# Kernel tuning notes

Measured on AMD Instinct MI355X. Metric: run time of the kernel, lower is better.

The kernel has to match this reference:

```python
import jax, jax.numpy as jnp
import numpy as np

N_NODES = 100000
N_RELS = 4
N_EDGES = 250000  # per relation
D = 128


def setup_inputs() -> dict:
    key = jax.random.key(0)
    ks = jax.random.split(key, 7)
    scale = 1.0 / np.sqrt(D)  # xavier-like scaling for stability
    x = jax.random.normal(ks[0], (N_NODES, D), dtype=jnp.float32)
    weight = jax.random.normal(ks[1], (N_RELS, D, D), dtype=jnp.float32) * scale
    conv_bias = jax.random.normal(ks[2], (N_RELS, D), dtype=jnp.float32) * 0.1
    loop_weight = jax.random.normal(ks[3], (D, D), dtype=jnp.float32) * scale
    node_bias = jax.random.normal(ks[4], (1, D), dtype=jnp.float32) * 0.1
    src = jax.random.randint(ks[5], (N_RELS, N_EDGES), 0, N_NODES)
    dst = jax.random.randint(ks[6], (N_RELS, N_EDGES), 0, N_NODES)
    return {"x": x, "weight": weight, "conv_bias": conv_bias,
            "loop_weight": loop_weight, "node_bias": node_bias,
            "src": src, "dst": dst}


def reference(x, weight, conv_bias, loop_weight, node_bias, src, dst):
    N = x.shape[0]

    def per_rel(s, d, W, b):
        # GraphConv(norm='right'): sum src feats into dst, divide by in-degree (clamped to 1),
        # then matmul weight (aggregate-first since in_feat == out_feat), add bias, activation.
        msg = jax.ops.segment_sum(x[s], d, num_segments=N)              # [N, D]
        deg = jax.ops.segment_sum(jnp.ones(s.shape, x.dtype), d, num_segments=N)
        h = (msg / jnp.maximum(deg, 1.0)[:, None]) @ W + b              # [N, D]
        return jax.nn.relu(h)

    hs = jax.vmap(per_rel)(src, dst, weight, conv_bias)                 # [R, N, D]
    h = hs.mean(axis=0)                                                 # HeteroGraphConv aggregate='mean'
    h = h * jax.nn.sigmoid(h)                                           # GLU(tile(h, 2)) == SiLU(h)
    h = h + x @ loop_weight + node_bias                                  # self-loop + ntype bias
    return jax.nn.relu(h)                                                # dropout=0 (eval)
```

## Files before the change

kernel.cpp:

```cpp
#include <hip/hip_runtime.h>
#include <hip/hip_bf16.h>

#define N_NODES 100000
#define N_RELS  4
#define N_EDGES 250000
#define TOTAL_E (N_RELS * N_EDGES)
#define NR      (N_RELS * N_NODES)
#define D       128

typedef __attribute__((ext_vector_type(8))) short bf16x8;
typedef __attribute__((ext_vector_type(4))) float f32x4;

__device__ __forceinline__ float b2f(short u) {
    unsigned int x = ((unsigned int)(unsigned short)u) << 16;
    return __builtin_bit_cast(float, x);
}
__device__ __forceinline__ unsigned short f2b(float f) {
    unsigned int u = __builtin_bit_cast(unsigned int, f);
    return (unsigned short)((u + 0x7fffu + ((u >> 16) & 1u)) >> 16);
}

#define PREP_X_BLKS 6250
#define PREP_W_BLKS 320
#define PREP_H_BLKS 3907
__global__ __launch_bounds__(256) void prep_kernel(
    const float* __restrict__ x, const float* __restrict__ weight,
    const float* __restrict__ loop_w, const int* __restrict__ dst,
    unsigned short* __restrict__ xb, unsigned short* __restrict__ wT,
    int* __restrict__ deg)
{
    int b = blockIdx.x, t = threadIdx.x;
    if (b < PREP_X_BLKS) {
        int i = b * 256 + t;
        float4 v0 = *reinterpret_cast<const float4*>(x + (size_t)i * 8);
        float4 v1 = *reinterpret_cast<const float4*>(x + (size_t)i * 8 + 4);
        bf16x8 o;
        o[0] = (short)f2b(v0.x); o[1] = (short)f2b(v0.y);
        o[2] = (short)f2b(v0.z); o[3] = (short)f2b(v0.w);
        o[4] = (short)f2b(v1.x); o[5] = (short)f2b(v1.y);
        o[6] = (short)f2b(v1.z); o[7] = (short)f2b(v1.w);
        *reinterpret_cast<bf16x8*>(xb + (size_t)i * 8) = o;
    } else if (b < PREP_X_BLKS + PREP_W_BLKS) {
        int i = (b - PREP_X_BLKS) * 256 + t;
        int mat = i >> 14;
        int n   = (i >> 7) & 127;
        int k   = i & 127;
        const float* srcm = (mat < 4) ? (weight + (size_t)mat * D * D) : loop_w;
        wT[i] = f2b(srcm[k * D + n]);
    } else {
        int i = (b - PREP_X_BLKS - PREP_W_BLKS) * 256 + t;
        if (i < TOTAL_E) {
            int rel = i / N_EDGES;
            atomicAdd(&deg[rel * N_NODES + dst[i]], 1);
        }
    }
}

__global__ __launch_bounds__(256) void scan1_kernel(
    const int* __restrict__ in, int* __restrict__ out,
    int* __restrict__ aux, int n)
{
    __shared__ int s[256];
    int t = threadIdx.x;
    int base = blockIdx.x * 1024 + t * 4;
    int v[4];
    int sum = 0;
    #pragma unroll
    for (int j = 0; j < 4; ++j) {
        v[j] = (base + j < n) ? in[base + j] : 0;
        sum += v[j];
    }
    s[t] = sum;
    for (int off = 1; off < 256; off <<= 1) {
        __syncthreads();
        int u = (t >= off) ? s[t - off] : 0;
        __syncthreads();
        s[t] += u;
    }
    __syncthreads();
    int excl = (t > 0) ? s[t - 1] : 0;
    #pragma unroll
    for (int j = 0; j < 4; ++j) {
        if (base + j < n) out[base + j] = excl;
        excl += v[j];
    }
    if (t == 255) aux[blockIdx.x] = s[255];
}

__global__ __launch_bounds__(256) void addoff2_kernel(
    int* __restrict__ off, int* __restrict__ cursor,
    const int* __restrict__ aux, int n)
{
    __shared__ int sred[256];
    int c = blockIdx.x, t = threadIdx.x;
    if (c == 0 && t == 0) off[NR] = TOTAL_E;
    int part = 0;
    for (int j = t; j < c; j += 256) part += aux[j];
    sred[t] = part;
    for (int o = 128; o > 0; o >>= 1) {
        __syncthreads();
        if (t < o) sred[t] += sred[t + o];
    }
    __syncthreads();
    int S = sred[0];
    int base = c * 1024 + t * 4;
    #pragma unroll
    for (int j = 0; j < 4; ++j) {
        int i = base + j;
        if (i < n) { int v = off[i] + S; off[i] = v; cursor[i] = v; }
    }
}

__global__ __launch_bounds__(256) void fill_kernel(
    const int* __restrict__ dst, const int* __restrict__ src,
    int* __restrict__ cursor, int* __restrict__ sorted_src, int total)
{
    int i = blockIdx.x * 256 + threadIdx.x;
    if (i >= total) return;
    int rel = i / N_EDGES;
    int pos = atomicAdd(&cursor[rel * N_NODES + dst[i]], 1);
    sorted_src[pos] = src[i];
}

__global__ __launch_bounds__(256) void fused_gemm_mfma(
    const unsigned short* __restrict__ xb,
    const unsigned short* __restrict__ wT,
    const float* __restrict__ conv_bias,
    const float* __restrict__ node_bias,
    const int* __restrict__ off,
    const int* __restrict__ sorted_src,
    float* __restrict__ out)
{
    __shared__ __align__(16) unsigned char sIn[32 * 256];

    const int tid  = threadIdx.x;
    const int row0 = blockIdx.x * 32;
    const int wid  = tid >> 6;
    const int lane = tid & 63;
    const int l15  = lane & 15;
    const int l4   = lane >> 4;
    const int swA  = (l15 & 7) << 4;

    const int gr  = tid >> 3;
    const int gc  = tid & 7;
    const int gsw = (gr & 7) << 4;

    f32x4 acc_mean[2][2];
    f32x4 acc_self[2][2];
    #pragma unroll
    for (int m = 0; m < 2; ++m)
        #pragma unroll
        for (int n = 0; n < 2; ++n)
            acc_mean[m][n] = (f32x4){0.f, 0.f, 0.f, 0.f};

    for (int phase = 0; phase < 4; ++phase) {
        __syncthreads();

        {
            int node = phase * N_NODES + row0 + gr;
            int beg  = off[node];
            int dgi  = off[node + 1] - beg;
            const int* sp = sorted_src + beg;
            const unsigned short* xcol = xb + gc * 16;

            float a[16];
            #pragma unroll
            for (int j = 0; j < 16; ++j) a[j] = 0.f;

            int e = 0;
            for (; e + 4 <= dgi; e += 4) {
                int s0 = sp[e], s1 = sp[e + 1], s2 = sp[e + 2], s3 = sp[e + 3];
                const bf16x8* p0 = reinterpret_cast<const bf16x8*>(xcol + (size_t)s0 * D);
                const bf16x8* p1 = reinterpret_cast<const bf16x8*>(xcol + (size_t)s1 * D);
                const bf16x8* p2 = reinterpret_cast<const bf16x8*>(xcol + (size_t)s2 * D);
                const bf16x8* p3 = reinterpret_cast<const bf16x8*>(xcol + (size_t)s3 * D);
                bf16x8 u0 = p0[0], w0 = p0[1];
                bf16x8 u1 = p1[0], w1 = p1[1];
                bf16x8 u2 = p2[0], w2 = p2[1];
                bf16x8 u3 = p3[0], w3 = p3[1];
                #pragma unroll
                for (int j = 0; j < 8; ++j) {
                    a[j]     += b2f(u0[j]) + b2f(u1[j]) + b2f(u2[j]) + b2f(u3[j]);
                    a[8 + j] += b2f(w0[j]) + b2f(w1[j]) + b2f(w2[j]) + b2f(w3[j]);
                }
            }
            for (; e < dgi; ++e) {
                const bf16x8* p = reinterpret_cast<const bf16x8*>(xcol + (size_t)sp[e] * D);
                bf16x8 u = p[0], w = p[1];
                #pragma unroll
                for (int j = 0; j < 8; ++j) {
                    a[j]     += b2f(u[j]);
                    a[8 + j] += b2f(w[j]);
                }
            }

            float scl = 1.0f / fmaxf((float)dgi, 1.0f);
            bf16x8 o0, o1;
            #pragma unroll
            for (int j = 0; j < 8; ++j) {
                o0[j] = (short)f2b(a[j] * scl);
                o1[j] = (short)f2b(a[8 + j] * scl);
            }
            int base = gr * 256;
            *reinterpret_cast<bf16x8*>(&sIn[base + ((gc * 32) ^ gsw)])      = o0;
            *reinterpret_cast<bf16x8*>(&sIn[base + ((gc * 32 + 16) ^ gsw)]) = o1;
        }
        __syncthreads();

        const unsigned short* wp = wT + (size_t)phase * D * D;
        f32x4 acc[2][2];
        #pragma unroll
        for (int m = 0; m < 2; ++m)
            #pragma unroll
            for (int n = 0; n < 2; ++n)
                acc[m][n] = (f32x4){0.f, 0.f, 0.f, 0.f};

        #pragma unroll
        for (int s = 0; s < 4; ++s) {
            int kb = s * 64 + l4 * 16;
            bf16x8 a0 = *reinterpret_cast<const bf16x8*>(
                &sIn[l15 * 256 + (kb ^ swA)]);
            bf16x8 a1 = *reinterpret_cast<const bf16x8*>(
                &sIn[(16 + l15) * 256 + (kb ^ swA)]);
            bf16x8 b0 = *reinterpret_cast<const bf16x8*>(
                wp + (wid * 32 + l15) * D + s * 32 + l4 * 8);
            bf16x8 b1 = *reinterpret_cast<const bf16x8*>(
                wp + (wid * 32 + 16 + l15) * D + s * 32 + l4 * 8);
            acc[0][0] = __builtin_amdgcn_mfma_f32_16x16x32_bf16(a0, b0, acc[0][0], 0, 0, 0);
            acc[0][1] = __builtin_amdgcn_mfma_f32_16x16x32_bf16(a0, b1, acc[0][1], 0, 0, 0);
            acc[1][0] = __builtin_amdgcn_mfma_f32_16x16x32_bf16(a1, b0, acc[1][0], 0, 0, 0);
            acc[1][1] = __builtin_amdgcn_mfma_f32_16x16x32_bf16(a1, b1, acc[1][1], 0, 0, 0);
        }

        float b0 = conv_bias[phase * D + wid * 32 + l15];
        float b1 = conv_bias[phase * D + wid * 32 + 16 + l15];
        #pragma unroll
        for (int m = 0; m < 2; ++m)
            #pragma unroll
            for (int j = 0; j < 4; ++j) {
                acc_mean[m][0][j] += 0.25f * fmaxf(acc[m][0][j] + b0, 0.f);
                acc_mean[m][1][j] += 0.25f * fmaxf(acc[m][1][j] + b1, 0.f);
            }
    }

    {
        const unsigned short* wp = wT + (size_t)4 * D * D;
        f32x4 acc[2][2];
        #pragma unroll
        for (int m = 0; m < 2; ++m)
            #pragma unroll
            for (int n = 0; n < 2; ++n)
                acc[m][n] = (f32x4){0.f, 0.f, 0.f, 0.f};

        #pragma unroll
        for (int s = 0; s < 4; ++s) {
            bf16x8 a0 = *reinterpret_cast<const bf16x8*>(
                xb + (size_t)(row0 + l15) * D + s * 32 + l4 * 8);
            bf16x8 a1 = *reinterpret_cast<const bf16x8*>(
                xb + (size_t)(row0 + 16 + l15) * D + s * 32 + l4 * 8);
            bf16x8 b0 = *reinterpret_cast<const bf16x8*>(
                wp + (wid * 32 + l15) * D + s * 32 + l4 * 8);
            bf16x8 b1 = *reinterpret_cast<const bf16x8*>(
                wp + (wid * 32 + 16 + l15) * D + s * 32 + l4 * 8);
            acc[0][0] = __builtin_amdgcn_mfma_f32_16x16x32_bf16(a0, b0, acc[0][0], 0, 0, 0);
            acc[0][1] = __builtin_amdgcn_mfma_f32_16x16x32_bf16(a0, b1, acc[0][1], 0, 0, 0);
            acc[1][0] = __builtin_amdgcn_mfma_f32_16x16x32_bf16(a1, b0, acc[1][0], 0, 0, 0);
            acc[1][1] = __builtin_amdgcn_mfma_f32_16x16x32_bf16(a1, b1, acc[1][1], 0, 0, 0);
        }
        float b0 = node_bias[wid * 32 + l15];
        float b1 = node_bias[wid * 32 + 16 + l15];
        #pragma unroll
        for (int m = 0; m < 2; ++m)
            #pragma unroll
            for (int j = 0; j < 4; ++j) {
                acc_self[m][0][j] = acc[m][0][j] + b0;
                acc_self[m][1][j] = acc[m][1][j] + b1;
            }
    }

    #pragma unroll
    for (int m = 0; m < 2; ++m)
        #pragma unroll
        for (int n = 0; n < 2; ++n)
            #pragma unroll
            for (int j = 0; j < 4; ++j) {
                float mn = acc_mean[m][n][j];
                float sl = mn / (1.0f + __expf(-mn));
                float v  = fmaxf(sl + acc_self[m][n][j], 0.f);
                int row = row0 + m * 16 + l4 * 4 + j;
                int col = wid * 32 + n * 16 + l15;
                out[(size_t)row * D + col] = v;
            }
}

extern "C" void kernel_launch(void* const* d_in, const int* in_sizes, int n_in,
                              void* d_out, int out_size, void* d_ws, size_t ws_size,
                              hipStream_t stream) {
    const float* x         = (const float*)d_in[0];
    const float* weight    = (const float*)d_in[1];
    const float* conv_bias = (const float*)d_in[2];
    const float* loop_w    = (const float*)d_in[3];
    const float* node_bias = (const float*)d_in[4];
    const int*   src       = (const int*)d_in[5];
    const int*   dst       = (const int*)d_in[6];
    float* out = (float*)d_out;

    char* w = (char*)d_ws;
    int* deg            = (int*)(w);
    int* off            = (int*)(w + 1600000);
    int* cursor         = (int*)(w + 3200008);
    int* aux            = (int*)(w + 4800008);
    int* sorted_src     = (int*)(w + 4802056);
    unsigned short* xb  = (unsigned short*)(w + 8802056);
    unsigned short* wT  = (unsigned short*)(w + 8802056 + (size_t)N_NODES * D * 2);

    const int SCAN_BLKS = (NR + 1023) / 1024;

    hipMemsetAsync(deg, 0, NR * sizeof(int), stream);
    prep_kernel<<<PREP_X_BLKS + PREP_W_BLKS + PREP_H_BLKS, 256, 0, stream>>>(
        x, weight, loop_w, dst, xb, wT, deg);
    scan1_kernel<<<SCAN_BLKS, 256, 0, stream>>>(deg, off, aux, NR);
    addoff2_kernel<<<SCAN_BLKS, 256, 0, stream>>>(off, cursor, aux, NR);
    fill_kernel<<<(TOTAL_E + 255) / 256, 256, 0, stream>>>(
        dst, src, cursor, sorted_src, TOTAL_E);
    fused_gemm_mfma<<<N_NODES / 32, 256, 0, stream>>>(
        xb, wT, conv_bias, node_bias, off, sorted_src, out);
}
```

Baseline: 356.9 us.

## Shrink fused GEMM to one wave per 16-row tile with hoisted offsets

The fused gather-plus-MFMA kernel now uses single-wavefront blocks, each handling 16 nodes instead of 32. Each lane gathers 32 columns of one node rather than 16, and that wave computes all 128 output columns with 8 MFMA accumulators. Offsets for all four relations are loaded up front. This creates twice as many, lighter blocks and makes the block barriers cheap, but each wave now loads every weight tile itself and needs more registers.

```diff
diff --git a/kernel.cpp b/kernel.cpp
--- a/kernel.cpp
+++ b/kernel.cpp
@@ -122,7 +122,7 @@
     sorted_src[pos] = src[i];
 }
 
-__global__ __launch_bounds__(256) void fused_gemm_mfma(
+__global__ __launch_bounds__(64) void fused_gemm_mfma(
     const unsigned short* __restrict__ xb,
     const unsigned short* __restrict__ wT,
     const float* __restrict__ conv_bias,
@@ -131,166 +131,147 @@
     const int* __restrict__ sorted_src,
     float* __restrict__ out)
 {
-    __shared__ __align__(16) unsigned char sIn[32 * 256];
-
-    const int tid  = threadIdx.x;
-    const int row0 = blockIdx.x * 32;
-    const int wid  = tid >> 6;
-    const int lane = tid & 63;
+    __shared__ __align__(16) unsigned char sIn[16 * 256];
+
+    const int lane = threadIdx.x;
+    const int row0 = blockIdx.x * 16;
     const int l15  = lane & 15;
     const int l4   = lane >> 4;
     const int swA  = (l15 & 7) << 4;
 
-    const int gr  = tid >> 3;
-    const int gc  = tid & 7;
+    const int gr  = lane >> 2;
+    const int gc  = lane & 3;
     const int gsw = (gr & 7) << 4;
 
-    f32x4 acc_mean[2][2];
-    f32x4 acc_self[2][2];
-    #pragma unroll
-    for (int m = 0; m < 2; ++m)
-        #pragma unroll
-        for (int n = 0; n < 2; ++n)
-            acc_mean[m][n] = (f32x4){0.f, 0.f, 0.f, 0.f};
+    int begs[4], ends[4];
+    #pragma unroll
+    for (int p = 0; p < 4; ++p) {
+        int node = p * N_NODES + row0 + gr;
+        begs[p] = off[node];
+        ends[p] = off[node + 1];
+    }
+
+    f32x4 acc_mean[8];
+    #pragma unroll
+    for (int n = 0; n < 8; ++n) acc_mean[n] = (f32x4){0.f, 0.f, 0.f, 0.f};
 
     for (int phase = 0; phase < 4; ++phase) {
         __syncthreads();
 
         {
-            int node = phase * N_NODES + row0 + gr;
-            int beg  = off[node];
-            int dgi  = off[node + 1] - beg;
-            const int* sp = sorted_src + beg;
-            const unsigned short* xcol = xb + gc * 16;
-
-            float a[16];
-            #pragma unroll
-            for (int j = 0; j < 16; ++j) a[j] = 0.f;
-
-            int e = 0;
-            for (; e + 4 <= dgi; e += 4) {
-                int s0 = sp[e], s1 = sp[e + 1], s2 = sp[e + 2], s3 = sp[e + 3];
+            int beg = begs[phase], end = ends[phase];
+            const unsigned short* xcol = xb + gc * 32;
+            float a[32];
+            #pragma unroll
+            for (int j = 0; j < 32; ++j) a[j] = 0.f;
+
+            int e = beg;
+            for (; e + 2 <= end; e += 2) {
+                int s0 = sorted_src[e], s1 = sorted_src[e + 1];
                 const bf16x8* p0 = reinterpret_cast<const bf16x8*>(xcol + (size_t)s0 * D);
                 const bf16x8* p1 = reinterpret_cast<const bf16x8*>(xcol + (size_t)s1 * D);
-                const bf16x8* p2 = reinterpret_cast<const bf16x8*>(xcol + (size_t)s2 * D);
-                const bf16x8* p3 = reinterpret_cast<const bf16x8*>(xcol + (size_t)s3 * D);
-                bf16x8 u0 = p0[0], w0 = p0[1];
-                bf16x8 u1 = p1[0], w1 = p1[1];
-                bf16x8 u2 = p2[0], w2 = p2[1];
-                bf16x8 u3 = p3[0], w3 = p3[1];
+                bf16x8 u0 = p0[0], u1 = p0[1], u2 = p0[2], u3 = p0[3];
+                bf16x8 v0 = p1[0], v1 = p1[1], v2 = p1[2], v3 = p1[3];
                 #pragma unroll
                 for (int j = 0; j < 8; ++j) {
-                    a[j]     += b2f(u0[j]) + b2f(u1[j]) + b2f(u2[j]) + b2f(u3[j]);
-                    a[8 + j] += b2f(w0[j]) + b2f(w1[j]) + b2f(w2[j]) + b2f(w3[j]);
+                    a[j]      += b2f(u0[j]) + b2f(v0[j]);
+                    a[8 + j]  += b2f(u1[j]) + b2f(v1[j]);
+                    a[16 + j] += b2f(u2[j]) + b2f(v2[j]);
+                    a[24 + j] += b2f(u3[j]) + b2f(v3[j]);
                 }
             }
-            for (; e < dgi; ++e) {
-                const bf16x8* p = reinterpret_cast<const bf16x8*>(xcol + (size_t)sp[e] * D);
-                bf16x8 u = p[0], w = p[1];
+            if (e < end) {
+                int s0 = sorted_src[e];
+                const bf16x8* p0 = reinterpret_cast<const bf16x8*>(xcol + (size_t)s0 * D);
+                bf16x8 u0 = p0[0], u1 = p0[1], u2 = p0[2], u3 = p0[3];
                 #pragma unroll
                 for (int j = 0; j < 8; ++j) {
-                    a[j]     += b2f(u[j]);
-                    a[8 + j] += b2f(w[j]);
+                    a[j]      += b2f(u0[j]);
+                    a[8 + j]  += b2f(u1[j]);
+                    a[16 + j] += b2f(u2[j]);
+                    a[24 + j] += b2f(u3[j]);
                 }
             }
 
-            float scl = 1.0f / fmaxf((float)dgi, 1.0f);
-            bf16x8 o0, o1;
-            #pragma unroll
-            for (int j = 0; j < 8; ++j) {
-                o0[j] = (short)f2b(a[j] * scl);
-                o1[j] = (short)f2b(a[8 + j] * scl);
-            }
-            int base = gr * 256;
-            *reinterpret_cast<bf16x8*>(&sIn[base + ((gc * 32) ^ gsw)])      = o0;
-            *reinterpret_cast<bf16x8*>(&sIn[base + ((gc * 32 + 16) ^ gsw)]) = o1;
+            float scl = 1.0f / fmaxf((float)(end - beg), 1.0f);
+            #pragma unroll
+            for (int q = 0; q < 4; ++q) {
+                bf16x8 o;
+                #pragma unroll
+                for (int j = 0; j < 8; ++j) o[j] = (short)f2b(a[q * 8 + j] * scl);
+                *reinterpret_cast<bf16x8*>(
+                    &sIn[gr * 256 + ((gc * 64 + q * 16) ^ gsw)]) = o;
+            }
         }
         __syncthreads();
 
         const unsigned short* wp = wT + (size_t)phase * D * D;
-        f32x4 acc[2][2];
-        #pragma unroll
-        for (int m = 0; m < 2; ++m)
-            #pragma unroll
-            for (int n = 0; n < 2; ++n)
-                acc[m][n] = (f32x4){0.f, 0.f, 0.f, 0.f};
+        float cb[8];
+        #pragma unroll
+        for (int n = 0; n < 8; ++n)
+            cb[n] = conv_bias[phase * D + n * 16 + l15];
+
+        f32x4 acc[8];
+        #pragma unroll
+        for (int n = 0; n < 8; ++n) acc[n] = (f32x4){0.f, 0.f, 0.f, 0.f};
 
         #pragma unroll
         for (int s = 0; s < 4; ++s) {
-            int kb = s * 64 + l4 * 16;
             bf16x8 a0 = *reinterpret_cast<const bf16x8*>(
-                &sIn[l15 * 256 + (kb ^ swA)]);
-            bf16x8 a1 = *reinterpret_cast<const bf16x8*>(
-                &sIn[(16 + l15) * 256 + (kb ^ swA)]);
-            bf16x8 b0 = *reinterpret_cast<const bf16x8*>(
-                wp + (wid * 32 + l15) * D + s * 32 + l4 * 8);
-            bf16x8 b1 = *reinterpret_cast<const bf16x8*>(
-                wp + (wid * 32 + 16 + l15) * D + s * 32 + l4 * 8);
-            acc[0][0] = __builtin_amdgcn_mfma_f32_16x16x32_bf16(a0, b0, acc[0][0], 0, 0, 0);
-            acc[0][1] = __builtin_amdgcn_mfma_f32_16x16x32_bf16(a0, b1, acc[0][1], 0, 0, 0);
-            acc[1][0] = __builtin_amdgcn_mfma_f32_16x16x32_bf16(a1, b0, acc[1][0], 0, 0, 0);
-            acc[1][1] = __builtin_amdgcn_mfma_f32_16x16x32_bf16(a1, b1, acc[1][1], 0, 0, 0);
-        }
-
-        float b0 = conv_bias[phase * D + wid * 32 + l15];
-        float b1 = conv_bias[phase * D + wid * 32 + 16 + l15];
-        #pragma unroll
-        for (int m = 0; m < 2; ++m)
-            #pragma unroll
-            for (int j = 0; j < 4; ++j) {
-                acc_mean[m][0][j] += 0.25f * fmaxf(acc[m][0][j] + b0, 0.f);
-                acc_mean[m][1][j] += 0.25f * fmaxf(acc[m][1][j] + b1, 0.f);
-            }
-    }
-
+                &sIn[l15 * 256 + ((s * 64 + l4 * 16) ^ swA)]);
+            #pragma unroll
+            for (int n = 0; n < 8; ++n) {
+                bf16x8 b0 = *reinterpret_cast<const bf16x8*>(
+                    wp + (n * 16 + l15) * D + s * 32 + l4 * 8);
+                acc[n] = __builtin_amdgcn_mfma_f32_16x16x32_bf16(a0, b0, acc[n], 0, 0, 0);
+            }
+        }
+
+        #pragma unroll
+        for (int n = 0; n < 8; ++n)
+            #pragma unroll
+            for (int j = 0; j < 4; ++j)
+                acc_mean[n][j] += 0.25f * fmaxf(acc[n][j] + cb[n], 0.f);
+    }
+
+    f32x4 acc_self[8];
     {
         const unsigned short* wp = wT + (size_t)4 * D * D;
-        f32x4 acc[2][2];
-        #pragma unroll
-        for (int m = 0; m < 2; ++m)
-            #pragma unroll
-            for (int n = 0; n < 2; ++n)
-                acc[m][n] = (f32x4){0.f, 0.f, 0.f, 0.f};
+        float nb[8];
+        #pragma unroll
+        for (int n = 0; n < 8; ++n) nb[n] = node_bias[n * 16 + l15];
+        #pragma unroll
+        for (int n = 0; n < 8; ++n) acc_self[n] = (f32x4){0.f, 0.f, 0.f, 0.f};
 
         #pragma unroll
         for (int s = 0; s < 4; ++s) {
             bf16x8 a0 = *reinterpret_cast<const bf16x8*>(
                 xb + (size_t)(row0 + l15) * D + s * 32 + l4 * 8);
-            bf16x8 a1 = *reinterpret_cast<const bf16x8*>(
-                xb + (size_t)(row0 + 16 + l15) * D + s * 32 + l4 * 8);
-            bf16x8 b0 = *reinterpret_cast<const bf16x8*>(
-                wp + (wid * 32 + l15) * D + s * 32 + l4 * 8);
-            bf16x8 b1 = *reinterpret_cast<const bf16x8*>(
-                wp + (wid * 32 + 16 + l15) * D + s * 32 + l4 * 8);
-            acc[0][0] = __builtin_amdgcn_mfma_f32_16x16x32_bf16(a0, b0, acc[0][0], 0, 0, 0);
-            acc[0][1] = __builtin_amdgcn_mfma_f32_16x16x32_bf16(a0, b1, acc[0][1], 0, 0, 0);
-            acc[1][0] = __builtin_amdgcn_mfma_f32_16x16x32_bf16(a1, b0, acc[1][0], 0, 0, 0);
-            acc[1][1] = __builtin_amdgcn_mfma_f32_16x16x32_bf16(a1, b1, acc[1][1], 0, 0, 0);
-        }
-        float b0 = node_bias[wid * 32 + l15];
-        float b1 = node_bias[wid * 32 + 16 + l15];
-        #pragma unroll
-        for (int m = 0; m < 2; ++m)
-            #pragma unroll
-            for (int j = 0; j < 4; ++j) {
-                acc_self[m][0][j] = acc[m][0][j] + b0;
-                acc_self[m][1][j] = acc[m][1][j] + b1;
-            }
-    }
-
-    #pragma unroll
-    for (int m = 0; m < 2; ++m)
-        #pragma unroll
-        for (int n = 0; n < 2; ++n)
-            #pragma unroll
-            for (int j = 0; j < 4; ++j) {
-                float mn = acc_mean[m][n][j];
-                float sl = mn / (1.0f + __expf(-mn));
-                float v  = fmaxf(sl + acc_self[m][n][j], 0.f);
-                int row = row0 + m * 16 + l4 * 4 + j;
-                int col = wid * 32 + n * 16 + l15;
-                out[(size_t)row * D + col] = v;
-            }
+            #pragma unroll
+            for (int n = 0; n < 8; ++n) {
+                bf16x8 b0 = *reinterpret_cast<const bf16x8*>(
+                    wp + (n * 16 + l15) * D + s * 32 + l4 * 8);
+                acc_self[n] = __builtin_amdgcn_mfma_f32_16x16x32_bf16(a0, b0, acc_self[n], 0, 0, 0);
+            }
+        }
+        #pragma unroll
+        for (int n = 0; n < 8; ++n)
+            #pragma unroll
+            for (int j = 0; j < 4; ++j)
+                acc_self[n][j] += nb[n];
+    }
+
+    #pragma unroll
+    for (int n = 0; n < 8; ++n)
+        #pragma unroll
+        for (int j = 0; j < 4; ++j) {
+            float mn = acc_mean[n][j];
+            float sl = mn / (1.0f + __expf(-mn));
+            float v  = fmaxf(sl + acc_self[n][j], 0.f);
+            int row = row0 + l4 * 4 + j;
+            int col = n * 16 + l15;
+            out[(size_t)row * D + col] = v;
+        }
 }
 
 extern "C" void kernel_launch(void* const* d_in, const int* in_sizes, int n_in,
@@ -323,6 +304,6 @@
     addoff2_kernel<<<SCAN_BLKS, 256, 0, stream>>>(off, cursor, aux, NR);
     fill_kernel<<<(TOTAL_E + 255) / 256, 256, 0, stream>>>(
         dst, src, cursor, sorted_src, TOTAL_E);
-    fused_gemm_mfma<<<N_NODES / 32, 256, 0, stream>>>(
+    fused_gemm_mfma<<<N_NODES / 16, 64, 0, stream>>>(
         xb, wT, conv_bias, node_bias, off, sorted_src, out);
 }
```

New measurement: 377.6 us. +5.8%, slower.

## Fuse CSR build into persistent grid-barrier kernel; gather all relations upfront

Applied to the files above, without the earlier changes.

Replaces the memset plus four preprocessing kernels with one persistent kernel of 1024 blocks that uses a software grid barrier between the degree count, scan, offset add and fill stages. This removes launch gaps and tail effects between small kernels. The main kernel now gathers all four relations' neighbour features in one interleaved loop, which raises memory-level parallelism. It then runs the four relation GEMMs from a 4x larger shared buffer without per-phase syncs. The grid barrier relies on all 1024 blocks being co-resident, which is a deadlock risk, and the larger LDS buffer and register arrays may reduce occupancy.

```diff
diff --git a/kernel.cpp b/kernel.cpp
--- a/kernel.cpp
+++ b/kernel.cpp
@@ -7,6 +7,8 @@
 #define TOTAL_E (N_RELS * N_EDGES)
 #define NR      (N_RELS * N_NODES)
 #define D       128
+#define CSR_BLKS 1024
+#define SCAN_BLKS 391
 
 typedef __attribute__((ext_vector_type(8))) short bf16x8;
 typedef __attribute__((ext_vector_type(4))) float f32x4;
@@ -20,18 +22,40 @@
     return (unsigned short)((u + 0x7fffu + ((u >> 16) & 1u)) >> 16);
 }
 
-#define PREP_X_BLKS 6250
-#define PREP_W_BLKS 320
-#define PREP_H_BLKS 3907
-__global__ __launch_bounds__(256) void prep_kernel(
+__device__ __forceinline__ void grid_barrier(int* cnt, int* gen) {
+    __syncthreads();
+    __threadfence();
+    if (threadIdx.x == 0) {
+        int my = __hip_atomic_load(gen, __ATOMIC_RELAXED, __HIP_MEMORY_SCOPE_AGENT);
+        int t  = __hip_atomic_fetch_add(cnt, 1, __ATOMIC_ACQ_REL, __HIP_MEMORY_SCOPE_AGENT);
+        if (t == CSR_BLKS - 1) {
+            __hip_atomic_store(cnt, 0, __ATOMIC_RELAXED, __HIP_MEMORY_SCOPE_AGENT);
+            __hip_atomic_fetch_add(gen, 1, __ATOMIC_RELEASE, __HIP_MEMORY_SCOPE_AGENT);
+        } else {
+            while (__hip_atomic_load(gen, __ATOMIC_ACQUIRE, __HIP_MEMORY_SCOPE_AGENT) == my)
+                __builtin_amdgcn_s_sleep(8);
+        }
+    }
+    __syncthreads();
+    __threadfence();
+}
+
+__global__ __launch_bounds__(256, 4) void csr_prep_kernel(
     const float* __restrict__ x, const float* __restrict__ weight,
-    const float* __restrict__ loop_w, const int* __restrict__ dst,
+    const float* __restrict__ loop_w, const int* __restrict__ src,
+    const int* __restrict__ dst,
     unsigned short* __restrict__ xb, unsigned short* __restrict__ wT,
-    int* __restrict__ deg)
+    int* __restrict__ deg, int* __restrict__ off, int* __restrict__ cursor,
+    int* __restrict__ aux, int* __restrict__ sorted_src,
+    int* __restrict__ bar_cnt, int* __restrict__ bar_gen)
 {
-    int b = blockIdx.x, t = threadIdx.x;
-    if (b < PREP_X_BLKS) {
-        int i = b * 256 + t;
+    const int t   = threadIdx.x;
+    const int gid = blockIdx.x * 256 + t;
+    const int NT  = CSR_BLKS * 256;
+    __shared__ int s[256];
+
+    for (int i = gid; i < NR; i += NT) deg[i] = 0;
+    for (int i = gid; i < N_NODES * D / 8; i += NT) {
         float4 v0 = *reinterpret_cast<const float4*>(x + (size_t)i * 8);
         float4 v1 = *reinterpret_cast<const float4*>(x + (size_t)i * 8 + 4);
         bf16x8 o;
@@ -40,86 +64,71 @@
         o[4] = (short)f2b(v1.x); o[5] = (short)f2b(v1.y);
         o[6] = (short)f2b(v1.z); o[7] = (short)f2b(v1.w);
         *reinterpret_cast<bf16x8*>(xb + (size_t)i * 8) = o;
-    } else if (b < PREP_X_BLKS + PREP_W_BLKS) {
-        int i = (b - PREP_X_BLKS) * 256 + t;
-        int mat = i >> 14;
-        int n   = (i >> 7) & 127;
-        int k   = i & 127;
+    }
+    for (int i = gid; i < 5 * D * D; i += NT) {
+        int mat = i >> 14, n = (i >> 7) & 127, k = i & 127;
         const float* srcm = (mat < 4) ? (weight + (size_t)mat * D * D) : loop_w;
         wT[i] = f2b(srcm[k * D + n]);
-    } else {
-        int i = (b - PREP_X_BLKS - PREP_W_BLKS) * 256 + t;
-        if (i < TOTAL_E) {
-            int rel = i / N_EDGES;
-            atomicAdd(&deg[rel * N_NODES + dst[i]], 1);
-        }
-    }
-}
-
-__global__ __launch_bounds__(256) void scan1_kernel(
-    const int* __restrict__ in, int* __restrict__ out,
-    int* __restrict__ aux, int n)
-{
-    __shared__ int s[256];
-    int t = threadIdx.x;
-    int base = blockIdx.x * 1024 + t * 4;
-    int v[4];
-    int sum = 0;
-    #pragma unroll
-    for (int j = 0; j < 4; ++j) {
-        v[j] = (base + j < n) ? in[base + j] : 0;
-        sum += v[j];
-    }
-    s[t] = sum;
-    for (int off = 1; off < 256; off <<= 1) {
+    }
+    grid_barrier(bar_cnt, bar_gen);
+
+    for (int i = gid; i < TOTAL_E; i += NT) {
+        int rel = i / N_EDGES;
+        atomicAdd(&deg[rel * N_NODES + dst[i]], 1);
+    }
+    grid_barrier(bar_cnt, bar_gen);
+
+    if (blockIdx.x < SCAN_BLKS) {
+        int base = blockIdx.x * 1024 + t * 4;
+        int v[4]; int sum = 0;
+        #pragma unroll
+        for (int j = 0; j < 4; ++j) {
+            v[j] = (base + j < NR) ? deg[base + j] : 0;
+            sum += v[j];
+        }
+        s[t] = sum;
+        for (int o = 1; o < 256; o <<= 1) {
+            __syncthreads();
+            int u = (t >= o) ? s[t - o] : 0;
+            __syncthreads();
+            s[t] += u;
+        }
         __syncthreads();
-        int u = (t >= off) ? s[t - off] : 0;
+        int excl = (t > 0) ? s[t - 1] : 0;
+        #pragma unroll
+        for (int j = 0; j < 4; ++j) {
+            if (base + j < NR) off[base + j] = excl;
+            excl += v[j];
+        }
+        if (t == 255) aux[blockIdx.x] = s[255];
+    }
+    grid_barrier(bar_cnt, bar_gen);
+
+    if (blockIdx.x < SCAN_BLKS) {
+        if (blockIdx.x == 0 && t == 0) off[NR] = TOTAL_E;
+        int part = 0;
+        for (int j = t; j < (int)blockIdx.x; j += 256) part += aux[j];
+        s[t] = part;
+        for (int o = 128; o > 0; o >>= 1) {
+            __syncthreads();
+            if (t < o) s[t] += s[t + o];
+        }
         __syncthreads();
-        s[t] += u;
-    }
-    __syncthreads();
-    int excl = (t > 0) ? s[t - 1] : 0;
-    #pragma unroll
-    for (int j = 0; j < 4; ++j) {
-        if (base + j < n) out[base + j] = excl;
-        excl += v[j];
-    }
-    if (t == 255) aux[blockIdx.x] = s[255];
-}
-
-__global__ __launch_bounds__(256) void addoff2_kernel(
-    int* __restrict__ off, int* __restrict__ cursor,
-    const int* __restrict__ aux, int n)
-{
-    __shared__ int sred[256];
-    int c = blockIdx.x, t = threadIdx.x;
-    if (c == 0 && t == 0) off[NR] = TOTAL_E;
-    int part = 0;
-    for (int j = t; j < c; j += 256) part += aux[j];
-    sred[t] = part;
-    for (int o = 128; o > 0; o >>= 1) {
-        __syncthreads();
-        if (t < o) sred[t] += sred[t + o];
-    }
-    __syncthreads();
-    int S = sred[0];
-    int base = c * 1024 + t * 4;
-    #pragma unroll
-    for (int j = 0; j < 4; ++j) {
-        int i = base + j;
-        if (i < n) { int v = off[i] + S; off[i] = v; cursor[i] = v; }
-    }
-}
-
-__global__ __launch_bounds__(256) void fill_kernel(
-    const int* __restrict__ dst, const int* __restrict__ src,
-    int* __restrict__ cursor, int* __restrict__ sorted_src, int total)
-{
-    int i = blockIdx.x * 256 + threadIdx.x;
-    if (i >= total) return;
-    int rel = i / N_EDGES;
-    int pos = atomicAdd(&cursor[rel * N_NODES + dst[i]], 1);
-    sorted_src[pos] = src[i];
+        int S = s[0];
+        int base = blockIdx.x * 1024 + t * 4;
+        #pragma unroll
+        for (int j = 0; j < 4; ++j) {
+            int i = base + j;
+            if (i < NR) { int v2 = off[i] + S; off[i] = v2; cursor[i] = v2; }
+        }
+    }
+    grid_barrier(bar_cnt, bar_gen);
+
+    for (int i = gid; i < TOTAL_E; i += NT) {
+        int rel = i / N_EDGES;
+        int pos = atomicAdd(&cursor[rel * N_NODES + dst[i]], 1);
+        sorted_src[pos] = src[i];
+    }
 }
 
 __global__ __launch_bounds__(256) void fused_gemm_mfma(
@@ -131,7 +140,7 @@
     const int* __restrict__ sorted_src,
     float* __restrict__ out)
 {
-    __shared__ __align__(16) unsigned char sIn[32 * 256];
+    __shared__ __align__(16) unsigned char sIn[4 * 32 * 256];
 
     const int tid  = threadIdx.x;
     const int row0 = blockIdx.x * 32;
@@ -145,68 +154,72 @@
     const int gc  = tid & 7;
     const int gsw = (gr & 7) << 4;
 
+    int begs[4], ends[4];
+    #pragma unroll
+    for (int p = 0; p < 4; ++p) {
+        int node = p * N_NODES + row0 + gr;
+        begs[p] = off[node];
+        ends[p] = off[node + 1];
+    }
+
+    {
+        const unsigned short* xcol = xb + gc * 16;
+        float a[4][16];
+        #pragma unroll
+        for (int p = 0; p < 4; ++p)
+            #pragma unroll
+            for (int j = 0; j < 16; ++j) a[p][j] = 0.f;
+
+        int e0 = begs[0], e1 = begs[1], e2 = begs[2], e3 = begs[3];
+        const int f0 = ends[0], f1 = ends[1], f2 = ends[2], f3 = ends[3];
+
+#define GATH(P, eP, fP)                                                        \
+        if (eP < fP) {                                                         \
+            int sn = sorted_src[eP];                                           \
+            const bf16x8* pp =                                                 \
+                reinterpret_cast<const bf16x8*>(xcol + (size_t)sn * D);        \
+            bf16x8 u = pp[0], v = pp[1];                                       \
+            _Pragma("unroll")                                                  \
+            for (int j = 0; j < 8; ++j) {                                      \
+                a[P][j]     += b2f(u[j]);                                      \
+                a[P][8 + j] += b2f(v[j]);                                      \
+            }                                                                  \
+            ++eP;                                                              \
+        }
+
+        while ((e0 < f0) || (e1 < f1) || (e2 < f2) || (e3 < f3)) {
+            GATH(0, e0, f0)
+            GATH(1, e1, f1)
+            GATH(2, e2, f2)
+            GATH(3, e3, f3)
+        }
+#undef GATH
+
+        #pragma unroll
+        for (int p = 0; p < 4; ++p) {
+            float scl = 1.0f / fmaxf((float)(ends[p] - begs[p]), 1.0f);
+            bf16x8 o0, o1;
+            #pragma unroll
+            for (int j = 0; j < 8; ++j) {
+                o0[j] = (short)f2b(a[p][j] * scl);
+                o1[j] = (short)f2b(a[p][8 + j] * scl);
+            }
+            int base = p * 8192 + gr * 256;
+            *reinterpret_cast<bf16x8*>(&sIn[base + ((gc * 32) ^ gsw)])      = o0;
+            *reinterpret_cast<bf16x8*>(&sIn[base + ((gc * 32 + 16) ^ gsw)]) = o1;
+        }
+    }
+    __syncthreads();
+
     f32x4 acc_mean[2][2];
-    f32x4 acc_self[2][2];
     #pragma unroll
     for (int m = 0; m < 2; ++m)
         #pragma unroll
         for (int n = 0; n < 2; ++n)
             acc_mean[m][n] = (f32x4){0.f, 0.f, 0.f, 0.f};
 
+    #pragma unroll
     for (int phase = 0; phase < 4; ++phase) {
-        __syncthreads();
-
-        {
-            int node = phase * N_NODES + row0 + gr;
-            int beg  = off[node];
-            int dgi  = off[node + 1] - beg;
-            const int* sp = sorted_src + beg;
-            const unsigned short* xcol = xb + gc * 16;
-
-            float a[16];
-            #pragma unroll
-            for (int j = 0; j < 16; ++j) a[j] = 0.f;
-
-            int e = 0;
-            for (; e + 4 <= dgi; e += 4) {
-                int s0 = sp[e], s1 = sp[e + 1], s2 = sp[e + 2], s3 = sp[e + 3];
-                const bf16x8* p0 = reinterpret_cast<const bf16x8*>(xcol + (size_t)s0 * D);
-                const bf16x8* p1 = reinterpret_cast<const bf16x8*>(xcol + (size_t)s1 * D);
-                const bf16x8* p2 = reinterpret_cast<const bf16x8*>(xcol + (size_t)s2 * D);
-                const bf16x8* p3 = reinterpret_cast<const bf16x8*>(xcol + (size_t)s3 * D);
-                bf16x8 u0 = p0[0], w0 = p0[1];
-                bf16x8 u1 = p1[0], w1 = p1[1];
-                bf16x8 u2 = p2[0], w2 = p2[1];
-                bf16x8 u3 = p3[0], w3 = p3[1];
-                #pragma unroll
-                for (int j = 0; j < 8; ++j) {
-                    a[j]     += b2f(u0[j]) + b2f(u1[j]) + b2f(u2[j]) + b2f(u3[j]);
-                    a[8 + j] += b2f(w0[j]) + b2f(w1[j]) + b2f(w2[j]) + b2f(w3[j]);
-                }
-            }
-            for (; e < dgi; ++e) {
-                const bf16x8* p = reinterpret_cast<const bf16x8*>(xcol + (size_t)sp[e] * D);
-                bf16x8 u = p[0], w = p[1];
-                #pragma unroll
-                for (int j = 0; j < 8; ++j) {
-                    a[j]     += b2f(u[j]);
-                    a[8 + j] += b2f(w[j]);
-                }
-            }
-
-            float scl = 1.0f / fmaxf((float)dgi, 1.0f);
-            bf16x8 o0, o1;
-            #pragma unroll
-            for (int j = 0; j < 8; ++j) {
-                o0[j] = (short)f2b(a[j] * scl);
-                o1[j] = (short)f2b(a[8 + j] * scl);
-            }
-            int base = gr * 256;
-            *reinterpret_cast<bf16x8*>(&sIn[base + ((gc * 32) ^ gsw)])      = o0;
-            *reinterpret_cast<bf16x8*>(&sIn[base + ((gc * 32 + 16) ^ gsw)]) = o1;
-        }
-        __syncthreads();
-
         const unsigned short* wp = wT + (size_t)phase * D * D;
         f32x4 acc[2][2];
         #pragma unroll
@@ -219,9 +232,9 @@
         for (int s = 0; s < 4; ++s) {
             int kb = s * 64 + l4 * 16;
             bf16x8 a0 = *reinterpret_cast<const bf16x8*>(
-                &sIn[l15 * 256 + (kb ^ swA)]);
+                &sIn[phase * 8192 + l15 * 256 + (kb ^ swA)]);
             bf16x8 a1 = *reinterpret_cast<const bf16x8*>(
-                &sIn[(16 + l15) * 256 + (kb ^ swA)]);
+                &sIn[phase * 8192 + (16 + l15) * 256 + (kb ^ swA)]);
             bf16x8 b0 = *reinterpret_cast<const bf16x8*>(
                 wp + (wid * 32 + l15) * D + s * 32 + l4 * 8);
             bf16x8 b1 = *reinterpret_cast<const bf16x8*>(
@@ -243,14 +256,14 @@
             }
     }
 
+    f32x4 acc_self[2][2];
     {
         const unsigned short* wp = wT + (size_t)4 * D * D;
-        f32x4 acc[2][2];
         #pragma unroll
         for (int m = 0; m < 2; ++m)
             #pragma unroll
             for (int n = 0; n < 2; ++n)
-                acc[m][n] = (f32x4){0.f, 0.f, 0.f, 0.f};
+                acc_self[m][n] = (f32x4){0.f, 0.f, 0.f, 0.f};
 
         #pragma unroll
         for (int s = 0; s < 4; ++s) {
@@ -262,10 +275,10 @@
                 wp + (wid * 32 + l15) * D + s * 32 + l4 * 8);
             bf16x8 b1 = *reinterpret_cast<const bf16x8*>(
                 wp + (wid * 32 + 16 + l15) * D + s * 32 + l4 * 8);
-            acc[0][0] = __builtin_amdgcn_mfma_f32_16x16x32_bf16(a0, b0, acc[0][0], 0, 0, 0);
-            acc[0][1] = __builtin_amdgcn_mfma_f32_16x16x32_bf16(a0, b1, acc[0][1], 0, 0, 0);
-            acc[1][0] = __builtin_amdgcn_mfma_f32_16x16x32_bf16(a1, b0, acc[1][0], 0, 0, 0);
-            acc[1][1] = __builtin_amdgcn_mfma_f32_16x16x32_bf16(a1, b1, acc[1][1], 0, 0, 0);
+            acc_self[0][0] = __builtin_amdgcn_mfma_f32_16x16x32_bf16(a0, b0, acc_self[0][0], 0, 0, 0);
+            acc_self[0][1] = __builtin_amdgcn_mfma_f32_16x16x32_bf16(a0, b1, acc_self[0][1], 0, 0, 0);
+            acc_self[1][0] = __builtin_amdgcn_mfma_f32_16x16x32_bf16(a1, b0, acc_self[1][0], 0, 0, 0);
+            acc_self[1][1] = __builtin_amdgcn_mfma_f32_16x16x32_bf16(a1, b1, acc_self[1][1], 0, 0, 0);
         }
         float b0 = node_bias[wid * 32 + l15];
         float b1 = node_bias[wid * 32 + 16 + l15];
@@ -273,8 +286,8 @@
         for (int m = 0; m < 2; ++m)
             #pragma unroll
             for (int j = 0; j < 4; ++j) {
-                acc_self[m][0][j] = acc[m][0][j] + b0;
-                acc_self[m][1][j] = acc[m][1][j] + b1;
+                acc_self[m][0][j] += b0;
+                acc_self[m][1][j] += b1;
             }
     }
 
@@ -310,19 +323,15 @@
     int* off            = (int*)(w + 1600000);
     int* cursor         = (int*)(w + 3200008);
     int* aux            = (int*)(w + 4800008);
+    int* bar            = (int*)(w + 4801800);
     int* sorted_src     = (int*)(w + 4802056);
     unsigned short* xb  = (unsigned short*)(w + 8802056);
     unsigned short* wT  = (unsigned short*)(w + 8802056 + (size_t)N_NODES * D * 2);
 
-    const int SCAN_BLKS = (NR + 1023) / 1024;
-
-    hipMemsetAsync(deg, 0, NR * sizeof(int), stream);
-    prep_kernel<<<PREP_X_BLKS + PREP_W_BLKS + PREP_H_BLKS, 256, 0, stream>>>(
-        x, weight, loop_w, dst, xb, wT, deg);
-    scan1_kernel<<<SCAN_BLKS, 256, 0, stream>>>(deg, off, aux, NR);
-    addoff2_kernel<<<SCAN_BLKS, 256, 0, stream>>>(off, cursor, aux, NR);
-    fill_kernel<<<(TOTAL_E + 255) / 256, 256, 0, stream>>>(
-        dst, src, cursor, sorted_src, TOTAL_E);
+    hipMemsetAsync(bar, 0, 8, stream);
+    csr_prep_kernel<<<CSR_BLKS, 256, 0, stream>>>(
+        x, weight, loop_w, src, dst, xb, wT,
+        deg, off, cursor, aux, sorted_src, bar, bar + 1);
     fused_gemm_mfma<<<N_NODES / 32, 256, 0, stream>>>(
         xb, wT, conv_bias, node_bias, off, sorted_src, out);
 }
```

Result: slower. 1.295 ms (+262.7%).
